# Kernel tuning notes

Hardware: AMD Instinct MI355X
Metric: run time of the kernel (lower is better)

## Reference

```python
import jax, jax.numpy as jnp
import numpy as np

B, T, N, D = 8, 24, 96, 32   # batch, timesteps, objects, per-object feature dim
H = 512                       # hidden_dim = cfg.MODEL.HIDDEN_SIZE * 2

def _linear_init(key, fan_in, fan_out):
    kw, kb = jax.random.split(key)
    s = 1.0 / np.sqrt(fan_in)
    W = jax.random.uniform(kw, (fan_in, fan_out), jnp.float32, -s, s)
    b = jax.random.uniform(kb, (fan_out,), jnp.float32, -s, s)
    return W, b

def setup_inputs() -> dict:
    key = jax.random.key(0)
    ks = jax.random.split(key, 8)
    x = jax.random.normal(ks[0], (B, T, N, D), jnp.float32)
    W_enc, b_enc = _linear_init(ks[1], 6 * D, H)
    W1, b1 = _linear_init(ks[2], H, H)
    W2, b2 = _linear_init(ks[3], H, H)
    W3, b3 = _linear_init(ks[4], H, H)
    Wd1, bd1 = _linear_init(ks[5], H, H)
    Wd2, bd2 = _linear_init(ks[6], H, D)
    return {"x": x, "W_enc": W_enc, "b_enc": b_enc, "W1": W1, "b1": b1,
            "W2": W2, "b2": b2, "W3": W3, "b3": b3,
            "Wd1": Wd1, "bd1": bd1, "Wd2": Wd2, "bd2": bd2}

def reference(x, W_enc, b_enc, W1, b1, W2, b2, W3, b3, Wd1, bd1, Wd2, bd2):
    relu = jax.nn.relu

    def int_net(s):  # s: [B, N, 3D] (concat of 3 past states)
        n = s.shape[1]
        e1 = jnp.broadcast_to(s[:, :, None, :], (s.shape[0], n, n, s.shape[-1]))
        e2 = jnp.broadcast_to(s[:, None, :, :], (s.shape[0], n, n, s.shape[-1]))
        pc = jnp.concatenate([e1, e2], axis=-1)          # [B, N, N, 6D]
        h = relu(pc @ W_enc + b_enc)
        h = relu(h @ W1 + b1)
        h = relu(h @ W2 + b2)
        emb = (h @ W3 + b3).mean(axis=2)                  # [B, N, H]
        return relu(emb @ Wd1 + bd1) @ Wd2 + bd2          # [B, N, D]

    z = jnp.zeros((B, N, D), jnp.float32)

    def step(carry, xt):  # xt: [B, N, D]
        p1, p2, p3 = carry
        exist = xt[:, :, 1:2]
        s = exist * xt + (1.0 - exist) * p3
        past = (p2, p3, s)
        out = int_net(jnp.concatenate(past, axis=-1))
        return past, out

    _, outs = jax.lax.scan(step, (z, z, z), jnp.swapaxes(x, 0, 1))  # outs: [T, B, N, D]
    return jnp.swapaxes(outs[:-1], 0, 1)  # [B, T-1, N, D]
```

## Files before the change

kernel.cpp:

```cpp
#include <hip/hip_runtime.h>

#define DEVI __device__ __forceinline__

typedef __bf16 bf16x8 __attribute__((ext_vector_type(8)));
typedef float  f32x4  __attribute__((ext_vector_type(4)));

static constexpr int Bb = 8, Tt = 24, Nn = 96, Dd = 32;
static constexpr int TO = 23;
static constexpr int TB = TO * Bb;
static constexpr int ROWS = TB * Nn;

DEVI unsigned short f2bf(float f) {
  union { float f; unsigned u; } v; v.f = f;
  unsigned r = v.u + 0x7FFFu + ((v.u >> 16) & 1u);
  return (unsigned short)(r >> 16);
}
DEVI float bf2f(unsigned short u) {
  union { unsigned u; float f; } v; v.u = (unsigned)u << 16; return v.f;
}

__global__ void pack_kernel(const float* __restrict__ W, unsigned short* __restrict__ dst,
                            int K, int N) {
  int p = blockIdx.x * 256 + threadIdx.x;
  if (p >= K * N) return;
  int j = p & 7, lane = (p >> 3) & 63, pb = p >> 9;
  int NB = N >> 4;
  int nb = pb % NB, kb = pb / NB;
  int k = kb * 32 + ((lane >> 4) << 3) + j;
  int n = nb * 16 + (lane & 15);
  dst[p] = f2bf(W[(size_t)k * N + n]);
}

__global__ void s3_kernel(const float* __restrict__ x, unsigned short* __restrict__ S3) {
  int tid = blockIdx.x * 256 + threadIdx.x;
  int b = tid / (Nn * Dd), n = (tid / Dd) % Nn, d = tid % Dd;
  auto idx = [&](int t, int k) { return ((size_t)((t * Bb + b) * Nn + n)) * 96 + k; };
  S3[idx(0, d)] = 0; S3[idx(0, 32 + d)] = 0; S3[idx(1, d)] = 0;
  float s = 0.f;
  for (int t = 0; t < TO; ++t) {
    const float* xr = x + ((size_t)(b * Tt + t) * Nn + n) * Dd;
    float e = xr[1];
    s = e * xr[d] + (1.f - e) * s;
    unsigned short sb = f2bf(s);
    S3[idx(t, 64 + d)] = sb;
    if (t + 1 < TO) S3[idx(t + 1, 32 + d)] = sb;
    if (t + 2 < TO) S3[idx(t + 2, d)] = sb;
  }
}

__global__ __launch_bounds__(512, 2) void uv_kernel(
    const unsigned short* __restrict__ S3, const unsigned short* __restrict__ WpE,
    const float* __restrict__ bE,
    unsigned short* __restrict__ U, unsigned short* __restrict__ V) {
  __shared__ unsigned short sS[96 * 104];
  int tid = threadIdx.x, lane = tid & 63, w = tid >> 6;
  int tb = blockIdx.x;
  const unsigned short* s3t = S3 + (size_t)tb * (96 * 96);
  for (int c = tid; c < 96 * 12; c += 512) {
    int j = c / 12, kc = (c % 12) * 8;
    *(bf16x8*)(sS + j * 104 + kc) = *(const bf16x8*)(s3t + j * 96 + kc);
  }
  __syncthreads();
#pragma unroll
  for (int half = 0; half < 2; ++half) {
    f32x4 acc[6][4];
#pragma unroll
    for (int m = 0; m < 6; ++m)
#pragma unroll
      for (int n = 0; n < 4; ++n) acc[m][n] = f32x4{0.f, 0.f, 0.f, 0.f};
#pragma unroll
    for (int kb = 0; kb < 3; ++kb) {
      bf16x8 a[6], b[4];
#pragma unroll
      for (int m = 0; m < 6; ++m) {
        int row = 16 * m + (lane & 15);
        a[m] = *(const bf16x8*)(sS + row * 104 + kb * 32 + ((lane >> 4) << 3));
      }
#pragma unroll
      for (int n = 0; n < 4; ++n)
        b[n] = *(const bf16x8*)(WpE + ((size_t)(((half * 3 + kb) * 32 + w * 4 + n) * 64 + lane) << 3));
#pragma unroll
      for (int n = 0; n < 4; ++n)
#pragma unroll
        for (int m = 0; m < 6; ++m)
          acc[m][n] = __builtin_amdgcn_mfma_f32_16x16x32_bf16(a[m], b[n], acc[m][n], 0, 0, 0);
    }
    unsigned short* dst = half ? V : U;
#pragma unroll
    for (int n = 0; n < 4; ++n) {
      int col = 64 * w + 16 * n + (lane & 15);
      float bias = half ? 0.f : bE[col];
#pragma unroll
      for (int m = 0; m < 6; ++m)
#pragma unroll
        for (int r = 0; r < 4; ++r) {
          int row = 16 * m + ((lane >> 4) << 2) + r;
          dst[((size_t)tb * 96 + row) * 512 + col] = f2bf(acc[m][n][r] + bias);
        }
    }
  }
}

template <int KB, int NFR>
DEVI void run_layer(const unsigned short* sA, const unsigned short* wp,
                    int NB, int nb0, int lane, int phase, f32x4 acc[6][NFR]) {
  const char* sab = (const char*)sA;
  const char* bb  = (const char*)wp + ((size_t)(nb0 * 64 + lane) << 4);
  const int kstride = NB << 10;
#pragma unroll 2
  for (int kb = 0; kb < KB; ++kb) {
    int kbp = (kb + phase) & (KB - 1);
    bf16x8 b[NFR];
#pragma unroll
    for (int n = 0; n < NFR; ++n)
      b[n] = *(const bf16x8*)(bb + kbp * kstride + (n << 10));
    bf16x8 a[6];
#pragma unroll
    for (int m = 0; m < 6; ++m) {
      int row = 16 * m + (lane & 15);
      int boff = (row * 1024 + kbp * 64 + ((lane >> 4) << 4)) ^ ((row & 15) << 4);
      a[m] = *(const bf16x8*)(sab + boff);
    }
#pragma unroll
    for (int n = 0; n < NFR; ++n)
#pragma unroll
      for (int m = 0; m < 6; ++m)
        acc[m][n] = __builtin_amdgcn_mfma_f32_16x16x32_bf16(a[m], b[n], acc[m][n], 0, 0, 0);
  }
}

template <int NFR>
DEVI void zacc(f32x4 (&acc)[6][NFR]) {
#pragma unroll
  for (int m = 0; m < 6; ++m)
#pragma unroll
    for (int n = 0; n < NFR; ++n) acc[m][n] = f32x4{0.f, 0.f, 0.f, 0.f};
}

template <bool RELU, int NFR>
DEVI void epilogue_to_lds(unsigned short* sA, const float* __restrict__ bias,
                          int w, int lane, f32x4 acc[6][NFR]) {
  float bn[NFR];
#pragma unroll
  for (int n = 0; n < NFR; ++n) bn[n] = bias[16 * NFR * w + 16 * n + (lane & 15)];
  __syncthreads();
  char* sab = (char*)sA;
#pragma unroll
  for (int m = 0; m < 6; ++m)
#pragma unroll
    for (int n = 0; n < NFR; ++n)
#pragma unroll
      for (int r = 0; r < 4; ++r) {
        float v = acc[m][n][r] + bn[n];
        if (RELU) v = fmaxf(v, 0.f);
        int row = 16 * m + ((lane >> 4) << 2) + r;
        int boff = (row * 1024 + (16 * NFR * w + 16 * n + (lane & 15)) * 2) ^ ((row & 15) << 4);
        *(unsigned short*)(sab + boff) = f2bf(v);
      }
  __syncthreads();
}

__global__ __launch_bounds__(1024)
__attribute__((amdgpu_waves_per_eu(4, 4))) void pair_kernel(
    const unsigned short* __restrict__ U, const unsigned short* __restrict__ V,
    const unsigned short* __restrict__ Wp1, const float* __restrict__ b1,
    const unsigned short* __restrict__ Wp2, const float* __restrict__ b2,
    unsigned short* __restrict__ hbar) {
  __shared__ unsigned short sA[96 * 512];
  int tid = threadIdx.x, lane = tid & 63, w = tid >> 6;
  int gid = blockIdx.x;
  int tb = gid / 96;
  int phase = gid & 15;
  const unsigned short* Up = U + (size_t)gid * 512;
  const unsigned short* Vp = V + (size_t)tb * (96 * 512);
  int kc = tid & 63;
  int j0 = tid >> 6;
  float u[8];
  {
    bf16x8 u8 = *(const bf16x8*)(Up + kc * 8);
#pragma unroll
    for (int l = 0; l < 8; ++l) u[l] = bf2f(((const unsigned short*)&u8)[l]);
  }
#pragma unroll
  for (int it = 0; it < 6; ++it) {
    int j = j0 + it * 16;
    bf16x8 v8 = *(const bf16x8*)(Vp + (size_t)j * 512 + kc * 8);
    unsigned short h[8];
#pragma unroll
    for (int l = 0; l < 8; ++l)
      h[l] = f2bf(fmaxf(u[l] + bf2f(((const unsigned short*)&v8)[l]), 0.f));
    int boff = (j * 1024 + kc * 16) ^ ((j & 15) << 4);
    *(bf16x8*)((char*)sA + boff) = *(bf16x8*)h;
  }
  __syncthreads();
  f32x4 acc[6][2];
  zacc(acc); run_layer<16, 2>(sA, Wp1, 32, w * 2, lane, phase, acc);
  epilogue_to_lds<true, 2>(sA, b1, w, lane, acc);
  zacc(acc); run_layer<16, 2>(sA, Wp2, 32, w * 2, lane, phase, acc);
  float p[2];
#pragma unroll
  for (int n = 0; n < 2; ++n) {
    float bn = b2[32 * w + 16 * n + (lane & 15)];
    float s = 0.f;
#pragma unroll
    for (int m = 0; m < 6; ++m)
#pragma unroll
      for (int r = 0; r < 4; ++r) s += fmaxf(acc[m][n][r] + bn, 0.f);
    p[n] = s;
  }
#pragma unroll
  for (int n = 0; n < 2; ++n) {
    p[n] += __shfl_xor(p[n], 16);
    p[n] += __shfl_xor(p[n], 32);
  }
  int g = lane >> 4;
  if (g < 2) {
    float sel = (g & 1) ? p[1] : p[0];
    hbar[(size_t)gid * 512 + 32 * w + (g & 1) * 16 + (lane & 15)] = f2bf(sel * (1.f / 96.f));
  }
}

__global__ __launch_bounds__(1024)
__attribute__((amdgpu_waves_per_eu(4, 4))) void decode_kernel(
    const unsigned short* __restrict__ hbar,
    const unsigned short* __restrict__ Wp3, const float* __restrict__ b3,
    const unsigned short* __restrict__ WpD1, const float* __restrict__ bd1,
    const unsigned short* __restrict__ WpD2, const float* __restrict__ bd2,
    float* __restrict__ out) {
  __shared__ unsigned short sA[96 * 512];
  int tid = threadIdx.x, lane = tid & 63, w = tid >> 6;
  int r0 = blockIdx.x * 96;
  int phase = blockIdx.x & 15;
  for (int c = tid; c < 96 * 64; c += 1024) {
    int j = c >> 6, kc = c & 63;
    bf16x8 v = *(const bf16x8*)(hbar + (size_t)(r0 + j) * 512 + kc * 8);
    int boff = (j * 1024 + kc * 16) ^ ((j & 15) << 4);
    *(bf16x8*)((char*)sA + boff) = v;
  }
  __syncthreads();
  f32x4 acc[6][2];
  zacc(acc); run_layer<16, 2>(sA, Wp3, 32, w * 2, lane, phase, acc);
  epilogue_to_lds<false, 2>(sA, b3, w, lane, acc);
  zacc(acc); run_layer<16, 2>(sA, WpD1, 32, w * 2, lane, phase, acc);
  epilogue_to_lds<true, 2>(sA, bd1, w, lane, acc);
  if (w == 0) {
    f32x4 acc2[6][2];
    zacc(acc2); run_layer<16, 2>(sA, WpD2, 2, 0, lane, phase, acc2);
#pragma unroll
    for (int n = 0; n < 2; ++n) {
      float bn = bd2[16 * n + (lane & 15)];
#pragma unroll
      for (int m = 0; m < 6; ++m)
#pragma unroll
        for (int r = 0; r < 4; ++r) {
          int row = 16 * m + ((lane >> 4) << 2) + r;
          int R = r0 + row;
          int t = R / 768, b = (R / 96) & 7, i = R % 96;
          out[(((size_t)b * TO + t) * 96 + i) * 32 + 16 * n + (lane & 15)] =
              acc2[m][n][r] + bn;
        }
    }
  }
}

extern "C" void kernel_launch(void* const* d_in, const int* in_sizes, int n_in,
                              void* d_out, int out_size, void* d_ws, size_t ws_size,
                              hipStream_t stream) {
  const float* x     = (const float*)d_in[0];
  const float* W_enc = (const float*)d_in[1];
  const float* b_enc = (const float*)d_in[2];
  const float* W1    = (const float*)d_in[3];
  const float* b1    = (const float*)d_in[4];
  const float* W2    = (const float*)d_in[5];
  const float* b2    = (const float*)d_in[6];
  const float* W3    = (const float*)d_in[7];
  const float* b3    = (const float*)d_in[8];
  const float* Wd1   = (const float*)d_in[9];
  const float* bd1   = (const float*)d_in[10];
  const float* Wd2   = (const float*)d_in[11];
  const float* bd2   = (const float*)d_in[12];
  float* out = (float*)d_out;

  char* ws = (char*)d_ws;
  size_t off = 0;
  auto alloc = [&](size_t bytes) {
    char* p = ws + off;
    off += (bytes + 255) & ~(size_t)255;
    return p;
  };
  unsigned short* S3    = (unsigned short*)alloc((size_t)TB * 96 * 96 * 2);
  unsigned short* Ub    = (unsigned short*)alloc((size_t)ROWS * 512 * 2);
  unsigned short* Vb    = (unsigned short*)alloc((size_t)ROWS * 512 * 2);
  unsigned short* hbar  = (unsigned short*)alloc((size_t)ROWS * 512 * 2);
  unsigned short* WpE   = (unsigned short*)alloc((size_t)192 * 512 * 2);
  unsigned short* Wp1p  = (unsigned short*)alloc((size_t)512 * 512 * 2);
  unsigned short* Wp2p  = (unsigned short*)alloc((size_t)512 * 512 * 2);
  unsigned short* Wp3p  = (unsigned short*)alloc((size_t)512 * 512 * 2);
  unsigned short* WpD1p = (unsigned short*)alloc((size_t)512 * 512 * 2);
  unsigned short* WpD2p = (unsigned short*)alloc((size_t)512 * 32 * 2);

  pack_kernel<<<(192 * 512) / 256, 256, 0, stream>>>(W_enc, WpE, 192, 512);
  pack_kernel<<<(512 * 512) / 256, 256, 0, stream>>>(W1, Wp1p, 512, 512);
  pack_kernel<<<(512 * 512) / 256, 256, 0, stream>>>(W2, Wp2p, 512, 512);
  pack_kernel<<<(512 * 512) / 256, 256, 0, stream>>>(W3, Wp3p, 512, 512);
  pack_kernel<<<(512 * 512) / 256, 256, 0, stream>>>(Wd1, WpD1p, 512, 512);
  pack_kernel<<<(512 * 32) / 256, 256, 0, stream>>>(Wd2, WpD2p, 512, 32);
  s3_kernel<<<96, 256, 0, stream>>>(x, S3);
  uv_kernel<<<TB, 512, 0, stream>>>(S3, WpE, b_enc, Ub, Vb);
  pair_kernel<<<ROWS, 1024, 0, stream>>>(Ub, Vb, Wp1p, b1, Wp2p, b2, hbar);
  decode_kernel<<<TB, 1024, 0, stream>>>(hbar, Wp3p, b3, WpD1p, bd1, WpD2p, bd2, out);
  (void)in_sizes; (void)n_in; (void)out_size; (void)ws_size;
}
```

Baseline: 1.575 ms.

## Switch MLP layers to 32x32x16 MFMA with transposed operand roles

Replaces the 16x16x32 bf16 MFMA tiling in the pair and decode kernels with 32x32x16 MFMA. Weights become the A operand, repacked by a new pack32 kernel, and activation rows from LDS become the B operand, so each wave computes 32 output columns across three 32-row fragments. Epilogues, the mean reduction and the output store are rewritten for the new accumulator layout, using vectorized bf16x4 LDS stores and native bf16 conversions. The goal is fewer MFMA issues and operand loads per FLOP, traded against a longer cross-lane shuffle reduction and a changed LDS access pattern.

```diff
diff --git a/kernel.cpp b/kernel.cpp
--- a/kernel.cpp
+++ b/kernel.cpp
@@ -3,7 +3,9 @@
 #define DEVI __device__ __forceinline__
 
 typedef __bf16 bf16x8 __attribute__((ext_vector_type(8)));
+typedef __bf16 bf16x4 __attribute__((ext_vector_type(4)));
 typedef float  f32x4  __attribute__((ext_vector_type(4)));
+typedef float  f32x16 __attribute__((ext_vector_type(16)));
 
 static constexpr int Bb = 8, Tt = 24, Nn = 96, Dd = 32;
 static constexpr int TO = 23;
@@ -14,9 +16,6 @@
   union { float f; unsigned u; } v; v.f = f;
   unsigned r = v.u + 0x7FFFu + ((v.u >> 16) & 1u);
   return (unsigned short)(r >> 16);
-}
-DEVI float bf2f(unsigned short u) {
-  union { unsigned u; float f; } v; v.u = (unsigned)u << 16; return v.f;
 }
 
 __global__ void pack_kernel(const float* __restrict__ W, unsigned short* __restrict__ dst,
@@ -28,6 +27,18 @@
   int nb = pb % NB, kb = pb / NB;
   int k = kb * 32 + ((lane >> 4) << 3) + j;
   int n = nb * 16 + (lane & 15);
+  dst[p] = f2bf(W[(size_t)k * N + n]);
+}
+
+__global__ void pack32_kernel(const float* __restrict__ W, unsigned short* __restrict__ dst,
+                              int K, int N) {
+  int p = blockIdx.x * 256 + threadIdx.x;
+  if (p >= K * N) return;
+  int jj = p & 7, lane = (p >> 3) & 63, pb = p >> 9;
+  int NB = N >> 5;
+  int nb = pb % NB, ks = pb / NB;
+  int k = ks * 16 + ((lane >> 5) << 3) + jj;
+  int n = nb * 32 + (lane & 31);
   dst[p] = f2bf(W[(size_t)k * N + n]);
 }
 
@@ -101,62 +112,65 @@
   }
 }
 
-template <int KB, int NFR>
-DEVI void run_layer(const unsigned short* sA, const unsigned short* wp,
-                    int NB, int nb0, int lane, int phase, f32x4 acc[6][NFR]) {
+template <int KS, int JF>
+DEVI void run_layer32(const unsigned short* sA, const unsigned short* wp,
+                      int NB, int nb0, int jf0, int lane, int phase, f32x16 (&acc)[JF]) {
   const char* sab = (const char*)sA;
-  const char* bb  = (const char*)wp + ((size_t)(nb0 * 64 + lane) << 4);
+  const char* ab  = (const char*)wp + ((size_t)(nb0 * 64 + lane) << 4);
   const int kstride = NB << 10;
+  const int xorv = (lane & 15) << 4;
+  const int hi16 = (lane >> 5) << 4;
+  int rb[JF];
+#pragma unroll
+  for (int f = 0; f < JF; ++f) rb[f] = ((jf0 + f) * 32 + (lane & 31)) << 10;
 #pragma unroll 2
-  for (int kb = 0; kb < KB; ++kb) {
-    int kbp = (kb + phase) & (KB - 1);
-    bf16x8 b[NFR];
-#pragma unroll
-    for (int n = 0; n < NFR; ++n)
-      b[n] = *(const bf16x8*)(bb + kbp * kstride + (n << 10));
-    bf16x8 a[6];
-#pragma unroll
-    for (int m = 0; m < 6; ++m) {
-      int row = 16 * m + (lane & 15);
-      int boff = (row * 1024 + kbp * 64 + ((lane >> 4) << 4)) ^ ((row & 15) << 4);
-      a[m] = *(const bf16x8*)(sab + boff);
-    }
-#pragma unroll
-    for (int n = 0; n < NFR; ++n)
-#pragma unroll
-      for (int m = 0; m < 6; ++m)
-        acc[m][n] = __builtin_amdgcn_mfma_f32_16x16x32_bf16(a[m], b[n], acc[m][n], 0, 0, 0);
-  }
-}
-
-template <int NFR>
-DEVI void zacc(f32x4 (&acc)[6][NFR]) {
-#pragma unroll
-  for (int m = 0; m < 6; ++m)
-#pragma unroll
-    for (int n = 0; n < NFR; ++n) acc[m][n] = f32x4{0.f, 0.f, 0.f, 0.f};
-}
-
-template <bool RELU, int NFR>
-DEVI void epilogue_to_lds(unsigned short* sA, const float* __restrict__ bias,
-                          int w, int lane, f32x4 acc[6][NFR]) {
-  float bn[NFR];
-#pragma unroll
-  for (int n = 0; n < NFR; ++n) bn[n] = bias[16 * NFR * w + 16 * n + (lane & 15)];
+  for (int ks = 0; ks < KS; ++ks) {
+    int ksp = (ks + phase) & (KS - 1);
+    bf16x8 a = *(const bf16x8*)(ab + (size_t)ksp * kstride);
+    int koff = (ksp * 32 + hi16) ^ xorv;
+    bf16x8 b[JF];
+#pragma unroll
+    for (int f = 0; f < JF; ++f) b[f] = *(const bf16x8*)(sab + rb[f] + koff);
+#pragma unroll
+    for (int f = 0; f < JF; ++f)
+      acc[f] = __builtin_amdgcn_mfma_f32_32x32x16_bf16(a, b[f], acc[f], 0, 0, 0);
+  }
+}
+
+template <int JF>
+DEVI void zacc32(f32x16 (&acc)[JF]) {
+#pragma unroll
+  for (int f = 0; f < JF; ++f)
+#pragma unroll
+    for (int i = 0; i < 16; ++i) acc[f][i] = 0.f;
+}
+
+template <bool RELU>
+DEVI void epilogue32(unsigned short* sA, const float* __restrict__ bias,
+                     int w, int lane, f32x16 (&acc)[3]) {
+  const int nb0 = 32 * w + ((lane >> 5) << 2);
+  f32x4 b4[4];
+#pragma unroll
+  for (int run = 0; run < 4; ++run) b4[run] = *(const f32x4*)(bias + nb0 + 8 * run);
   __syncthreads();
   char* sab = (char*)sA;
-#pragma unroll
-  for (int m = 0; m < 6; ++m)
-#pragma unroll
-    for (int n = 0; n < NFR; ++n)
-#pragma unroll
-      for (int r = 0; r < 4; ++r) {
-        float v = acc[m][n][r] + bn[n];
+  const int xorv = (lane & 15) << 4;
+  const int nbyte0 = nb0 * 2;
+#pragma unroll
+  for (int f = 0; f < 3; ++f) {
+    int rowb = (f * 32 + (lane & 31)) << 10;
+#pragma unroll
+    for (int run = 0; run < 4; ++run) {
+      bf16x4 h;
+#pragma unroll
+      for (int i = 0; i < 4; ++i) {
+        float v = acc[f][4 * run + i] + b4[run][i];
         if (RELU) v = fmaxf(v, 0.f);
-        int row = 16 * m + ((lane >> 4) << 2) + r;
-        int boff = (row * 1024 + (16 * NFR * w + 16 * n + (lane & 15)) * 2) ^ ((row & 15) << 4);
-        *(unsigned short*)(sab + boff) = f2bf(v);
+        h[i] = (__bf16)v;
       }
+      *(bf16x4*)(sab + rowb + ((nbyte0 + 16 * run) ^ xorv)) = h;
+    }
+  }
   __syncthreads();
 }
 
@@ -170,7 +184,7 @@
   int tid = threadIdx.x, lane = tid & 63, w = tid >> 6;
   int gid = blockIdx.x;
   int tb = gid / 96;
-  int phase = gid & 15;
+  int phase = gid & 31;
   const unsigned short* Up = U + (size_t)gid * 512;
   const unsigned short* Vp = V + (size_t)tb * (96 * 512);
   int kc = tid & 63;
@@ -179,44 +193,52 @@
   {
     bf16x8 u8 = *(const bf16x8*)(Up + kc * 8);
 #pragma unroll
-    for (int l = 0; l < 8; ++l) u[l] = bf2f(((const unsigned short*)&u8)[l]);
+    for (int l = 0; l < 8; ++l) u[l] = (float)u8[l];
   }
 #pragma unroll
   for (int it = 0; it < 6; ++it) {
     int j = j0 + it * 16;
     bf16x8 v8 = *(const bf16x8*)(Vp + (size_t)j * 512 + kc * 8);
-    unsigned short h[8];
+    bf16x8 h8;
 #pragma unroll
     for (int l = 0; l < 8; ++l)
-      h[l] = f2bf(fmaxf(u[l] + bf2f(((const unsigned short*)&v8)[l]), 0.f));
+      h8[l] = (__bf16)fmaxf(u[l] + (float)v8[l], 0.f);
     int boff = (j * 1024 + kc * 16) ^ ((j & 15) << 4);
-    *(bf16x8*)((char*)sA + boff) = *(bf16x8*)h;
-  }
-  __syncthreads();
-  f32x4 acc[6][2];
-  zacc(acc); run_layer<16, 2>(sA, Wp1, 32, w * 2, lane, phase, acc);
-  epilogue_to_lds<true, 2>(sA, b1, w, lane, acc);
-  zacc(acc); run_layer<16, 2>(sA, Wp2, 32, w * 2, lane, phase, acc);
-  float p[2];
-#pragma unroll
-  for (int n = 0; n < 2; ++n) {
-    float bn = b2[32 * w + 16 * n + (lane & 15)];
-    float s = 0.f;
-#pragma unroll
-    for (int m = 0; m < 6; ++m)
-#pragma unroll
-      for (int r = 0; r < 4; ++r) s += fmaxf(acc[m][n][r] + bn, 0.f);
-    p[n] = s;
-  }
-#pragma unroll
-  for (int n = 0; n < 2; ++n) {
-    p[n] += __shfl_xor(p[n], 16);
-    p[n] += __shfl_xor(p[n], 32);
-  }
-  int g = lane >> 4;
-  if (g < 2) {
-    float sel = (g & 1) ? p[1] : p[0];
-    hbar[(size_t)gid * 512 + 32 * w + (g & 1) * 16 + (lane & 15)] = f2bf(sel * (1.f / 96.f));
+    *(bf16x8*)((char*)sA + boff) = h8;
+  }
+  __syncthreads();
+  f32x16 acc[3];
+  zacc32(acc); run_layer32<32, 3>(sA, Wp1, 16, w, 0, lane, phase, acc);
+  epilogue32<true>(sA, b1, w, lane, acc);
+  zacc32(acc); run_layer32<32, 3>(sA, Wp2, 16, w, 0, lane, phase, acc);
+  const int nb0 = 32 * w + ((lane >> 5) << 2);
+  float p[16];
+#pragma unroll
+  for (int run = 0; run < 4; ++run) {
+    f32x4 b4 = *(const f32x4*)(b2 + nb0 + 8 * run);
+#pragma unroll
+    for (int i = 0; i < 4; ++i) {
+      int r = 4 * run + i;
+      p[r] = fmaxf(acc[0][r] + b4[i], 0.f) + fmaxf(acc[1][r] + b4[i], 0.f) +
+             fmaxf(acc[2][r] + b4[i], 0.f);
+    }
+  }
+#pragma unroll
+  for (int r = 0; r < 16; ++r) {
+    p[r] += __shfl_xor(p[r], 1);
+    p[r] += __shfl_xor(p[r], 2);
+    p[r] += __shfl_xor(p[r], 4);
+    p[r] += __shfl_xor(p[r], 8);
+    p[r] += __shfl_xor(p[r], 16);
+  }
+  if ((lane & 31) == 0) {
+#pragma unroll
+    for (int run = 0; run < 4; ++run) {
+      bf16x4 hv;
+#pragma unroll
+      for (int i = 0; i < 4; ++i) hv[i] = (__bf16)(p[4 * run + i] * (1.f / 96.f));
+      *(bf16x4*)((char*)hbar + ((size_t)gid * 512 + nb0 + 8 * run) * 2) = hv;
+    }
   }
 }
 
@@ -230,7 +252,7 @@
   __shared__ unsigned short sA[96 * 512];
   int tid = threadIdx.x, lane = tid & 63, w = tid >> 6;
   int r0 = blockIdx.x * 96;
-  int phase = blockIdx.x & 15;
+  int phase = blockIdx.x & 31;
   for (int c = tid; c < 96 * 64; c += 1024) {
     int j = c >> 6, kc = c & 63;
     bf16x8 v = *(const bf16x8*)(hbar + (size_t)(r0 + j) * 512 + kc * 8);
@@ -238,27 +260,27 @@
     *(bf16x8*)((char*)sA + boff) = v;
   }
   __syncthreads();
-  f32x4 acc[6][2];
-  zacc(acc); run_layer<16, 2>(sA, Wp3, 32, w * 2, lane, phase, acc);
-  epilogue_to_lds<false, 2>(sA, b3, w, lane, acc);
-  zacc(acc); run_layer<16, 2>(sA, WpD1, 32, w * 2, lane, phase, acc);
-  epilogue_to_lds<true, 2>(sA, bd1, w, lane, acc);
-  if (w == 0) {
-    f32x4 acc2[6][2];
-    zacc(acc2); run_layer<16, 2>(sA, WpD2, 2, 0, lane, phase, acc2);
-#pragma unroll
-    for (int n = 0; n < 2; ++n) {
-      float bn = bd2[16 * n + (lane & 15)];
-#pragma unroll
-      for (int m = 0; m < 6; ++m)
-#pragma unroll
-        for (int r = 0; r < 4; ++r) {
-          int row = 16 * m + ((lane >> 4) << 2) + r;
-          int R = r0 + row;
-          int t = R / 768, b = (R / 96) & 7, i = R % 96;
-          out[(((size_t)b * TO + t) * 96 + i) * 32 + 16 * n + (lane & 15)] =
-              acc2[m][n][r] + bn;
-        }
+  f32x16 acc[3];
+  zacc32(acc); run_layer32<32, 3>(sA, Wp3, 16, w, 0, lane, phase, acc);
+  epilogue32<false>(sA, b3, w, lane, acc);
+  zacc32(acc); run_layer32<32, 3>(sA, WpD1, 16, w, 0, lane, phase, acc);
+  epilogue32<true>(sA, bd1, w, lane, acc);
+  if (w < 3) {
+    f32x16 a2[1];
+    zacc32(a2);
+    run_layer32<32, 1>(sA, WpD2, 1, 0, w, lane, phase, a2);
+    int j = 32 * w + (lane & 31);
+    int R = r0 + j;
+    int t = R / 768, b = (R / 96) & 7, i = R % 96;
+    float* ob = out + (((size_t)b * TO + t) * 96 + i) * 32;
+    int hi4 = (lane >> 5) << 2;
+#pragma unroll
+    for (int run = 0; run < 4; ++run) {
+      f32x4 b4 = *(const f32x4*)(bd2 + hi4 + 8 * run);
+      f32x4 o;
+#pragma unroll
+      for (int i2 = 0; i2 < 4; ++i2) o[i2] = a2[0][4 * run + i2] + b4[i2];
+      *(f32x4*)(ob + hi4 + 8 * run) = o;
     }
   }
 }
@@ -300,11 +322,11 @@
   unsigned short* WpD2p = (unsigned short*)alloc((size_t)512 * 32 * 2);
 
   pack_kernel<<<(192 * 512) / 256, 256, 0, stream>>>(W_enc, WpE, 192, 512);
-  pack_kernel<<<(512 * 512) / 256, 256, 0, stream>>>(W1, Wp1p, 512, 512);
-  pack_kernel<<<(512 * 512) / 256, 256, 0, stream>>>(W2, Wp2p, 512, 512);
-  pack_kernel<<<(512 * 512) / 256, 256, 0, stream>>>(W3, Wp3p, 512, 512);
-  pack_kernel<<<(512 * 512) / 256, 256, 0, stream>>>(Wd1, WpD1p, 512, 512);
-  pack_kernel<<<(512 * 32) / 256, 256, 0, stream>>>(Wd2, WpD2p, 512, 32);
+  pack32_kernel<<<(512 * 512) / 256, 256, 0, stream>>>(W1, Wp1p, 512, 512);
+  pack32_kernel<<<(512 * 512) / 256, 256, 0, stream>>>(W2, Wp2p, 512, 512);
+  pack32_kernel<<<(512 * 512) / 256, 256, 0, stream>>>(W3, Wp3p, 512, 512);
+  pack32_kernel<<<(512 * 512) / 256, 256, 0, stream>>>(Wd1, WpD1p, 512, 512);
+  pack32_kernel<<<(512 * 32) / 256, 256, 0, stream>>>(Wd2, WpD2p, 512, 32);
   s3_kernel<<<96, 256, 0, stream>>>(x, S3);
   uv_kernel<<<TB, 512, 0, stream>>>(S3, WpE, b_enc, Ub, Vb);
   pair_kernel<<<ROWS, 1024, 0, stream>>>(Ub, Vb, Wp1p, b1, Wp2p, b2, hbar);
```

Measured after the change: 1.847 ms. 17.3% more time.
